# Optimization experiments

Measured on AMD Instinct MI355X. Metric: run time of the kernel, lower is better.

## Reference

```python
import jax, jax.numpy as jnp
import numpy as np

D_IN = 2048
D_SAE = 32768
K = 64


def setup_inputs() -> dict:
    key = jax.random.key(0)
    k1, k2, k3 = jax.random.split(key, 3)
    x = jax.random.normal(k1, (4096, D_IN), dtype=jnp.float32)
    # kaiming-uniform-style init
    bound_enc = float(np.sqrt(6.0 / D_IN))
    W_enc = jax.random.uniform(k2, (D_SAE, D_IN), jnp.float32, -bound_enc, bound_enc)
    bound_dec = float(np.sqrt(6.0 / D_SAE))
    W_dec = jax.random.uniform(k3, (D_IN, D_SAE), jnp.float32, -bound_dec, bound_dec)
    # normalize_decoder: unit-norm columns of W_dec
    norms = jnp.clip(jnp.linalg.norm(W_dec, axis=0, keepdims=True), 1e-8, None)
    W_dec = W_dec / norms
    b_enc = jnp.zeros((D_SAE,), jnp.float32)
    b_dec = jnp.zeros((D_IN,), jnp.float32)
    return {"x": x, "W_enc": W_enc, "b_enc": b_enc, "W_dec": W_dec, "b_dec": b_dec}


def _topk_activate(pre_acts):
    # pre_acts: [N, d_sae] -> dense sparse activations with K nonzeros/row
    vals, idx = jax.lax.top_k(pre_acts, K)          # [N, K]
    vals = jax.nn.relu(vals)
    rows = jnp.arange(pre_acts.shape[0])[:, None]   # [N, 1]
    return jnp.zeros_like(pre_acts).at[rows, idx].set(vals)


def reference(x, W_enc, b_enc, W_dec, b_dec):
    # encode: activation(W_enc @ (x - b_dec) + b_enc)
    pre_acts = (x - b_dec) @ W_enc.T + b_enc        # [N, d_sae]
    h = _topk_activate(pre_acts)
    # decode
    x_hat = h @ W_dec.T + b_dec                     # [N, d_in]
    recon_loss = jnp.mean((x_hat - x) ** 2)
    loss = recon_loss  # topk: sparsity_loss == 0
    return (x_hat, h, loss)
```

## Files before the change

kernel.cpp:

```cpp
#include <hip/hip_runtime.h>
#include <stdint.h>

#define D_IN   2048
#define D_SAE  32768
#define NROWS  4096
#define TOPK   64
#define CAND_CAP 320
#define BMAX   96
#define CV_E   0.02f
#define TAU_COEF 0.0796875f
#define BINW   0.03125f

typedef __attribute__((ext_vector_type(4)))  float f32x4;
typedef __attribute__((ext_vector_type(8)))  short short8;
typedef __attribute__((ext_vector_type(4)))  unsigned short u16x4;
typedef __attribute__((ext_vector_type(8)))  unsigned short u16x8;

__device__ __forceinline__ unsigned short f2bf(float f){
  unsigned int u = __float_as_uint(f);
  u = (u + 0x7FFFu + ((u >> 16) & 1u)) >> 16;
  return (unsigned short)u;
}
__device__ __forceinline__ float bf2f(unsigned short h){
  return __uint_as_float(((unsigned int)h) << 16);
}
__device__ __forceinline__ void async16(const unsigned short* g, unsigned short* l){
  __builtin_amdgcn_global_load_lds(
      (const __attribute__((address_space(1))) unsigned int*)g,
      (__attribute__((address_space(3))) unsigned int*)l,
      16, 0, 0);
}

__global__ void __launch_bounds__(256) k_prep(
    const float* __restrict__ x, const float* __restrict__ b_dec,
    const float* __restrict__ W_enc, const float* __restrict__ wdec,
    unsigned short* __restrict__ xbf, float* __restrict__ tau,
    int* __restrict__ cnt, unsigned short* __restrict__ wencb,
    unsigned short* __restrict__ wdt)
{
  __shared__ float tile[64][65];
  const int t = threadIdx.x;
  const int bid = blockIdx.x;
  if (bid < NROWS){
    float* red = &tile[0][0];
    const int n = bid;
    const f32x4* xr = (const f32x4*)(x + (size_t)n*D_IN);
    const f32x4* br = (const f32x4*)b_dec;
    u16x4* xo = (u16x4*)(xbf + (size_t)n*D_IN);
    float s = 0.f;
#pragma unroll
    for (int i=0;i<2;i++){
      const int p = t + 256*i;
      const f32x4 v = xr[p], b = br[p];
      f32x4 d; u16x4 r4;
#pragma unroll
      for (int j=0;j<4;j++){ d[j] = v[j]-b[j]; r4[j] = f2bf(d[j]); s = fmaf(d[j],d[j],s); }
      xo[p] = r4;
    }
    red[t] = s; __syncthreads();
    for (int o=128;o>0;o>>=1){ if (t<o) red[t] += red[t+o]; __syncthreads(); }
    if (t==0){ tau[n] = TAU_COEF * sqrtf(red[0]); cnt[n] = 0; }
  } else if (bid < NROWS + 32768){
    const int i = (bid - NROWS)*256 + t;
    const f32x4 v0 = ((const f32x4*)W_enc)[2*i];
    const f32x4 v1 = ((const f32x4*)W_enc)[2*i+1];
    u16x8 r;
#pragma unroll
    for (int j=0;j<4;j++){ r[j] = f2bf(v0[j]); r[j+4] = f2bf(v1[j]); }
    ((u16x8*)wencb)[i] = r;
  } else {
    const int tb = bid - (NROWS + 32768);
    const int j0 = (tb & 511)*64;
    const int i0 = (tb >> 9)*64;
    const int r = t >> 2, cq = (t & 3) * 16;
    const float* src = wdec + (size_t)(i0 + r)*D_SAE + j0 + cq;
#pragma unroll
    for (int k=0;k<4;k++){
      const f32x4 v = ((const f32x4*)src)[k];
#pragma unroll
      for (int e=0;e<4;e++) tile[r][cq + 4*k + e] = v[e];
    }
    __syncthreads();
    u16x8 o0, o1;
#pragma unroll
    for (int e=0;e<8;e++){
      o0[e] = f2bf(tile[cq + e][r]);
      o1[e] = f2bf(tile[cq + 8 + e][r]);
    }
    unsigned short* dst = wdt + (size_t)(j0 + r)*D_IN + i0 + cq;
    ((u16x8*)dst)[0] = o0;
    ((u16x8*)dst)[1] = o1;
  }
}

__global__ void __launch_bounds__(256) k_gemm(
    const unsigned short* __restrict__ A,
    const unsigned short* __restrict__ B,
    const float* __restrict__ b_enc,
    const float* __restrict__ tau,
    int* __restrict__ cnt, int* __restrict__ ci, float* __restrict__ cv)
{
  __shared__ unsigned short As[128*64];
  __shared__ unsigned short Bs[128*64];
  const int tid = threadIdx.x;
  const int w = tid >> 6, l = tid & 63;
  const int bm = blockIdx.x, bn = blockIdx.y;
  const size_t brow = (size_t)bm*128, bcol = (size_t)bn*128;
  const int wr = w >> 1, wc = w & 1;
  const int lr = l >> 3;
  const int lg = (l & 7) ^ lr;
  const int fr = l & 15, fq = l >> 4;
  const int fx = fr & 7;
  f32x4 acc[4][4] = {};
  const unsigned short* Ab = A + (brow + 8*w + lr)*D_IN + lg*8;
  const unsigned short* Bb = B + (bcol + 8*w + lr)*D_IN + lg*8;
  for (int kt = 0; kt < D_IN; kt += 64){
    __syncthreads();
#pragma unroll
    for (int c=0;c<4;c++){
      async16(Ab + (size_t)(32*c)*D_IN + kt, &As[c*2048 + w*512]);
      async16(Bb + (size_t)(32*c)*D_IN + kt, &Bs[c*2048 + w*512]);
    }
    __syncthreads();
    short8 af[4][2], bf[4][2];
#pragma unroll
    for (int m=0;m<4;m++)
#pragma unroll
      for (int kk=0;kk<2;kk++)
        af[m][kk] = *(const short8*)&As[(wr*64 + m*16 + fr)*64 + (((kk*4+fq) ^ fx)*8)];
#pragma unroll
    for (int n=0;n<4;n++)
#pragma unroll
      for (int kk=0;kk<2;kk++)
        bf[n][kk] = *(const short8*)&Bs[(wc*64 + n*16 + fr)*64 + (((kk*4+fq) ^ fx)*8)];
#pragma unroll
    for (int kk=0;kk<2;kk++)
#pragma unroll
      for (int m=0;m<4;m++)
#pragma unroll
        for (int n=0;n<4;n++)
          asm("v_mfma_f32_16x16x32_bf16 %0, %1, %2, %0" : "+v"(acc[m][n]) : "v"(af[m][kk]), "v"(bf[n][kk]));
  }
  asm volatile("s_nop 7\n\ts_nop 7" ::: "memory");
#pragma unroll
  for (int n=0;n<4;n++){
    const int col = (int)bcol + wc*64 + n*16 + fr;
    const float be = b_enc[col];
#pragma unroll
    for (int m=0;m<4;m++){
      const int row0 = (int)brow + wr*64 + m*16 + fq*4;
#pragma unroll
      for (int r=0;r<4;r++){
        const float v = acc[m][n][r] + be;
        const int row = row0 + r;
        if (v > tau[row]){
          const int pos = atomicAdd(&cnt[row], 1);
          if (pos < CAND_CAP){
            ci[(size_t)row*CAND_CAP + pos] = col;
            cv[(size_t)row*CAND_CAP + pos] = v;
          }
        }
      }
    }
  }
}

__global__ void __launch_bounds__(256) k_rescore(
    const float* __restrict__ x, const float* __restrict__ b_dec,
    const float* __restrict__ W, const float* __restrict__ b_enc,
    const float* __restrict__ tau, const int* __restrict__ cnt,
    const int* __restrict__ ci, const float* __restrict__ cv,
    const unsigned short* __restrict__ wdt,
    float* __restrict__ h, float* __restrict__ xhat, double* __restrict__ part)
{
  __shared__ f32x4 xa[D_IN/4];
  __shared__ float sval[CAND_CAP];
  __shared__ int   sidx[CAND_CAP];
  __shared__ unsigned hist[256];
  __shared__ unsigned tsuf[256];
  __shared__ float osv[TOPK];
  __shared__ int   osi[TOPK];
  __shared__ float exv[BMAX];
  __shared__ int   exi[BMAX];
  __shared__ int   blist[BMAX];
  __shared__ int   m1c, m2c, sbin;
  const int n = blockIdx.x, t = threadIdx.x, w = t>>6, l = t&63;

  {
    const f32x4* xr = (const f32x4*)(x + (size_t)n*D_IN);
    const f32x4* br = (const f32x4*)b_dec;
    for (int i=t;i<D_IN/4;i+=256){
      f32x4 v = xr[i], b = br[i], d;
      d[0]=v[0]-b[0]; d[1]=v[1]-b[1]; d[2]=v[2]-b[2]; d[3]=v[3]-b[3];
      xa[i] = d;
    }
  }
  {
    f32x4* hr = (f32x4*)(h + (size_t)n*D_SAE);
    const f32x4 z = {0.f,0.f,0.f,0.f};
#pragma unroll
    for (int i=0;i<32;i++) __builtin_nontemporal_store(z, hr + t + 256*i);
  }
  if (t < TOPK){ osv[t] = 0.f; osi[t] = 0; }
  hist[t] = 0u;
  if (t == 0){ m1c = 0; m2c = 0; sbin = 0; }
  int cn = cnt[n]; cn = cn < CAND_CAP ? cn : CAND_CAP;
  const float tn = tau[n];
  __syncthreads();
  for (int c=t; c<cn; c+=256){
    const float v = cv[(size_t)n*CAND_CAP + c];
    sval[c] = v;
    sidx[c] = ci[(size_t)n*CAND_CAP + c];
    int b = (int)((v - tn)*32.f); b = b<0?0:(b>255?255:b);
    atomicAdd(&hist[b], 1u);
  }
  __syncthreads();

  if (cn <= TOPK){
    for (int c=t; c<cn; c+=256){
      const int p = atomicAdd(&m1c, 1);
      osv[p] = sval[c]; osi[p] = sidx[c];
    }
    __syncthreads();
  } else {
    tsuf[t] = hist[t]; __syncthreads();
    for (int off=1; off<256; off<<=1){
      unsigned v = tsuf[t] + ((t+off<256)? tsuf[t+off] : 0u);
      __syncthreads();
      tsuf[t] = v;
      __syncthreads();
    }
    if (tsuf[t] >= (unsigned)TOPK) atomicMax(&sbin, t);
    __syncthreads();
    const int bT = sbin;
    const float THI = tn + (float)(bT+1)*BINW + 2.f*CV_E;
    const float TLO = tn + (float)bT*BINW     - 2.f*CV_E;
    for (int c=t; c<cn; c+=256){
      const float v = sval[c];
      if (v > THI){
        const int p = atomicAdd(&m1c, 1);
        osv[p] = v; osi[p] = sidx[c];
      } else if (v >= TLO){
        const int p = atomicAdd(&m2c, 1);
        if (p < BMAX) blist[p] = c;
      }
    }
    __syncthreads();
    const int m1 = m1c;
    const int m2 = m2c < BMAX ? m2c : BMAX;
    for (int c0 = w*2; c0 < m2; c0 += 8){
      const int c1 = c0 + 1;
      const int i0 = sidx[blist[c0]];
      const int i1 = (c1 < m2) ? sidx[blist[c1]] : i0;
      const f32x4* w0 = (const f32x4*)(W + (size_t)i0*D_IN);
      const f32x4* w1 = (const f32x4*)(W + (size_t)i1*D_IN);
      f32x4 a0 = {0.f,0.f,0.f,0.f}, a1 = {0.f,0.f,0.f,0.f};
#pragma unroll
      for (int e=0;e<8;e++){
        const int p = l + e*64;
        const f32x4 xv = xa[p];
        const f32x4 wv0 = w0[p];
        const f32x4 wv1 = w1[p];
#pragma unroll
        for (int j=0;j<4;j++) a0[j] = fmaf(xv[j], wv0[j], a0[j]);
#pragma unroll
        for (int j=0;j<4;j++) a1[j] = fmaf(xv[j], wv1[j], a1[j]);
      }
      float s0 = (a0[0]+a0[1]) + (a0[2]+a0[3]);
      float s1 = (a1[0]+a1[1]) + (a1[2]+a1[3]);
#pragma unroll
      for (int off=32; off>0; off>>=1){
        s0 += __shfl_down(s0, off);
        s1 += __shfl_down(s1, off);
      }
      if (l==0){
        exv[c0] = s0 + b_enc[i0]; exi[c0] = i0;
        if (c1 < m2){ exv[c1] = s1 + b_enc[i1]; exi[c1] = i1; }
      }
    }
    __syncthreads();
    if (w==0){
      const int need = TOPK - m1;
      for (int k=0;k<need;k++){
        float bv = -2.0e30f; int bi = 0x7FFFFFFF; int bp = -1;
        for (int c=l; c<m2; c+=64){
          const float v = exv[c]; const int idx = exi[c];
          if (v > bv || (v == bv && idx < bi)){ bv = v; bi = idx; bp = c; }
        }
#pragma unroll
        for (int off=32; off>0; off>>=1){
          const float ovv = __shfl_down(bv, off);
          const int   oii = __shfl_down(bi, off);
          const int   opp = __shfl_down(bp, off);
          if (ovv > bv || (ovv == bv && oii < bi)){ bv=ovv; bi=oii; bp=opp; }
        }
        bv = __shfl(bv, 0); bi = __shfl(bi, 0); bp = __shfl(bp, 0);
        if (l==0 && bp >= 0){
          osv[m1+k] = bv; osi[m1+k] = bi;
          exv[bp] = -3.0e30f;
        }
      }
    }
    __syncthreads();
  }
  if (t < TOPK){
    const float v = osv[t];
    if (v > 0.f) h[(size_t)n*D_SAE + osi[t]] = v;
  }
  __syncthreads();
  {
    const int d0 = t*8;
    float s[8] = {0.f,0.f,0.f,0.f,0.f,0.f,0.f,0.f};
    for (int k=0;k<TOPK;k++){
      const float v = osv[k];
      const u16x8 wv = *(const u16x8*)(wdt + (size_t)osi[k]*D_IN + d0);
#pragma unroll
      for (int j=0;j<8;j++) s[j] = fmaf(v, bf2f(wv[j]), s[j]);
    }
    const float* xaf = (const float*)xa;
    const f32x4 b0 = ((const f32x4*)b_dec)[t*2];
    const f32x4 b1 = ((const f32x4*)b_dec)[t*2+1];
    f32x4 o0, o1;
#pragma unroll
    for (int j=0;j<4;j++){ o0[j] = s[j] + b0[j]; o1[j] = s[j+4] + b1[j]; }
    float* xo = xhat + (size_t)n*D_IN + d0;
    ((f32x4*)xo)[0] = o0; ((f32x4*)xo)[1] = o1;
    float sq = 0.f;
#pragma unroll
    for (int j=0;j<8;j++){ const float d = s[j] - xaf[d0+j]; sq = fmaf(d,d,sq); }
    __syncthreads();
    sval[t] = sq; __syncthreads();
    for (int o=128;o>0;o>>=1){ if (t<o) sval[t] += sval[t+o]; __syncthreads(); }
    if (t==0) part[n] = (double)sval[0];
  }
}

__global__ void k_loss(const double* __restrict__ part, float* __restrict__ out){
  __shared__ double red[256];
  const int t = threadIdx.x;
  double a = 0.0;
  for (int i=t;i<NROWS;i+=256) a += part[i];
  red[t] = a; __syncthreads();
  for (int s=128;s>0;s>>=1){ if (t<s) red[t]+=red[t+s]; __syncthreads(); }
  if (t==0) out[0] = (float)(red[0] / (double)((size_t)NROWS * D_IN));
}

extern "C" void kernel_launch(void* const* d_in, const int* in_sizes, int n_in,
                              void* d_out, int out_size, void* d_ws, size_t ws_size,
                              hipStream_t stream)
{
  const float* x     = (const float*)d_in[0];
  const float* W_enc = (const float*)d_in[1];
  const float* b_enc = (const float*)d_in[2];
  const float* W_dec = (const float*)d_in[3];
  const float* b_dec = (const float*)d_in[4];

  float* xhat = (float*)d_out;
  float* h    = xhat + (size_t)NROWS*D_IN;
  float* loss = h + (size_t)NROWS*D_SAE;

  char* ws = (char*)d_ws;
  unsigned short* xbf   = (unsigned short*)(ws);
  unsigned short* wencb = (unsigned short*)(ws + 16777216);
  unsigned short* wdt   = (unsigned short*)(ws + 150994944);
  int*   ci   = (int*)  (ws + 285212672);
  float* cv   = (float*)(ws + 290455552);
  int*   cnt  = (int*)  (ws + 295698432);
  float* tau  = (float*)(ws + 295714816);
  double* part= (double*)(ws + 295731200);

  k_prep      <<<dim3(53248),   dim3(256), 0, stream>>>(x, b_dec, W_enc, W_dec, xbf, tau, cnt, wencb, wdt);
  k_gemm      <<<dim3(32,256),  dim3(256), 0, stream>>>(xbf, wencb, b_enc, tau, cnt, ci, cv);
  k_rescore   <<<dim3(4096),    dim3(256), 0, stream>>>(x, b_dec, W_enc, b_enc, tau, cnt, ci, cv, wdt, h, xhat, part);
  k_loss      <<<dim3(1),       dim3(256), 0, stream>>>(part, loss);
}
```

Before: 1.029 ms.

## Enlarge encoder GEMM tile to 256x256 with double-buffered async LDS pipeline

The encoder GEMM moves from 128x128 tiles with 4 waves to 256x256 tiles with 8 waves. LDS is double-buffered, and the global-to-LDS loads for the next K-steps are interleaved with the MFMA phases using explicit waitcnt and barrier instructions, plus priority raising around the MFMAs. The aim is to overlap memory latency with compute and raise arithmetic intensity per tile. In exchange it adds register pressure from 32 accumulators per wave and more LDS use, and fewer blocks will fit per CU.

```diff
diff --git a/kernel.cpp b/kernel.cpp
--- a/kernel.cpp
+++ b/kernel.cpp
@@ -10,6 +10,7 @@
 #define CV_E   0.02f
 #define TAU_COEF 0.0796875f
 #define BINW   0.03125f
+#define NT_K   32
 
 typedef __attribute__((ext_vector_type(4)))  float f32x4;
 typedef __attribute__((ext_vector_type(8)))  short short8;
@@ -93,62 +94,90 @@
   }
 }
 
-__global__ void __launch_bounds__(256) k_gemm(
+__global__ void __launch_bounds__(512) k_gemm(
     const unsigned short* __restrict__ A,
     const unsigned short* __restrict__ B,
     const float* __restrict__ b_enc,
     const float* __restrict__ tau,
     int* __restrict__ cnt, int* __restrict__ ci, float* __restrict__ cv)
 {
-  __shared__ unsigned short As[128*64];
-  __shared__ unsigned short Bs[128*64];
+  __shared__ unsigned short Abuf[2][2][8192];
+  __shared__ unsigned short Bbuf[2][2][8192];
   const int tid = threadIdx.x;
   const int w = tid >> 6, l = tid & 63;
   const int bm = blockIdx.x, bn = blockIdx.y;
-  const size_t brow = (size_t)bm*128, bcol = (size_t)bn*128;
-  const int wr = w >> 1, wc = w & 1;
-  const int lr = l >> 3;
-  const int lg = (l & 7) ^ lr;
+  const int brow = bm*256, bcol = bn*256;
+  const int wm = w >> 2, wn = w & 3;
   const int fr = l & 15, fq = l >> 4;
   const int fx = fr & 7;
-  f32x4 acc[4][4] = {};
-  const unsigned short* Ab = A + (brow + 8*w + lr)*D_IN + lg*8;
-  const unsigned short* Bb = B + (bcol + 8*w + lr)*D_IN + lg*8;
-  for (int kt = 0; kt < D_IN; kt += 64){
-    __syncthreads();
-#pragma unroll
-    for (int c=0;c<4;c++){
-      async16(Ab + (size_t)(32*c)*D_IN + kt, &As[c*2048 + w*512]);
-      async16(Bb + (size_t)(32*c)*D_IN + kt, &Bs[c*2048 + w*512]);
-    }
-    __syncthreads();
-    short8 af[4][2], bf[4][2];
-#pragma unroll
-    for (int m=0;m<4;m++)
+  const int r0 = tid >> 3;
+  const int g0 = (tid & 7) ^ (r0 & 7);
+  const unsigned short* Asrc = A + (size_t)(brow + r0)*D_IN + g0*8;
+  const unsigned short* Bsrc = B + (size_t)(bcol + r0)*D_IN + g0*8;
+  f32x4 acc[8][4] = {};
+
+#define SA(h, T) do{ \
+    async16(Asrc + (size_t)((h)*128     )*D_IN + (T)*64, &Abuf[(T)&1][h][w*512]); \
+    async16(Asrc + (size_t)((h)*128 + 64)*D_IN + (T)*64, &Abuf[(T)&1][h][4096 + w*512]); }while(0)
+#define SB(h, T) do{ \
+    async16(Bsrc + (size_t)((h)*128     )*D_IN + (T)*64, &Bbuf[(T)&1][h][w*512]); \
+    async16(Bsrc + (size_t)((h)*128 + 64)*D_IN + (T)*64, &Bbuf[(T)&1][h][4096 + w*512]); }while(0)
+
+  SA(0,0); SA(1,0); SB(0,0); SB(1,0);
+  SB(0,1); SB(1,1);
+  asm volatile("s_waitcnt vmcnt(0)" ::: "memory");
+  asm volatile("s_barrier" ::: "memory");
+
+  for (int T = 0; T < NT_K; ++T){
+    const unsigned short* Ah = Abuf[T&1][wm];
+    const unsigned short* Bh = Bbuf[T&1][wn>>1];
+    short8 bfr[4][2];
+#pragma unroll
+    for (int q=0;q<4;q++){
+      short8 af[2][2];
+      if (q==0){
+#pragma unroll
+        for (int n=0;n<4;n++)
+#pragma unroll
+          for (int kk=0;kk<2;kk++)
+            bfr[n][kk] = *(const short8*)&Bh[((wn&1)*64 + n*16 + fr)*64 + (((kk*4+fq) ^ fx)*8)];
+      }
+#pragma unroll
+      for (int mm=0;mm<2;mm++)
+#pragma unroll
+        for (int kk=0;kk<2;kk++)
+          af[mm][kk] = *(const short8*)&Ah[((q*2+mm)*16 + fr)*64 + (((kk*4+fq) ^ fx)*8)];
+      if (q==0 && T+1 < NT_K) SA(0, T+1);
+      if (q==1 && T+1 < NT_K) SA(1, T+1);
+      if (q==2 && T+2 < NT_K) SB(0, T+2);
+      if (q==3 && T+2 < NT_K) SB(1, T+2);
+      asm volatile("s_barrier" ::: "memory");
+      __builtin_amdgcn_s_setprio(1);
 #pragma unroll
       for (int kk=0;kk<2;kk++)
-        af[m][kk] = *(const short8*)&As[(wr*64 + m*16 + fr)*64 + (((kk*4+fq) ^ fx)*8)];
-#pragma unroll
-    for (int n=0;n<4;n++)
-#pragma unroll
-      for (int kk=0;kk<2;kk++)
-        bf[n][kk] = *(const short8*)&Bs[(wc*64 + n*16 + fr)*64 + (((kk*4+fq) ^ fx)*8)];
-#pragma unroll
-    for (int kk=0;kk<2;kk++)
-#pragma unroll
-      for (int m=0;m<4;m++)
-#pragma unroll
-        for (int n=0;n<4;n++)
-          asm("v_mfma_f32_16x16x32_bf16 %0, %1, %2, %0" : "+v"(acc[m][n]) : "v"(af[m][kk]), "v"(bf[n][kk]));
-  }
+#pragma unroll
+        for (int mm=0;mm<2;mm++)
+#pragma unroll
+          for (int n=0;n<4;n++)
+            asm("v_mfma_f32_16x16x32_bf16 %0, %1, %2, %0" : "+v"(acc[q*2+mm][n]) : "v"(af[mm][kk]), "v"(bfr[n][kk]));
+      __builtin_amdgcn_s_setprio(0);
+      if (q==3){
+        if (T < NT_K-2) asm volatile("s_waitcnt vmcnt(4)" ::: "memory");
+        else            asm volatile("s_waitcnt vmcnt(0)" ::: "memory");
+      }
+      asm volatile("s_barrier" ::: "memory");
+    }
+  }
+#undef SA
+#undef SB
   asm volatile("s_nop 7\n\ts_nop 7" ::: "memory");
 #pragma unroll
   for (int n=0;n<4;n++){
-    const int col = (int)bcol + wc*64 + n*16 + fr;
+    const int col = bcol + wn*64 + n*16 + fr;
     const float be = b_enc[col];
 #pragma unroll
-    for (int m=0;m<4;m++){
-      const int row0 = (int)brow + wr*64 + m*16 + fq*4;
+    for (int m=0;m<8;m++){
+      const int row0 = brow + wm*128 + m*16 + fq*4;
 #pragma unroll
       for (int r=0;r<4;r++){
         const float v = acc[m][n][r] + be;
@@ -370,7 +399,7 @@
   double* part= (double*)(ws + 295731200);
 
   k_prep      <<<dim3(53248),   dim3(256), 0, stream>>>(x, b_dec, W_enc, W_dec, xbf, tau, cnt, wencb, wdt);
-  k_gemm      <<<dim3(32,256),  dim3(256), 0, stream>>>(xbf, wencb, b_enc, tau, cnt, ci, cv);
+  k_gemm      <<<dim3(16,128),  dim3(512), 0, stream>>>(xbf, wencb, b_enc, tau, cnt, ci, cv);
   k_rescore   <<<dim3(4096),    dim3(256), 0, stream>>>(x, b_dec, W_enc, b_enc, tau, cnt, ci, cv, wdt, h, xhat, part);
   k_loss      <<<dim3(1),       dim3(256), 0, stream>>>(part, loss);
 }
```

Result: slower. 1.412 ms (+37.2%).
